# Kernel optimization log

Hardware: AMD Instinct MI355X
Metric: run time of the kernel (lower is better)

The kernel has to match this reference:

```python
import jax, jax.numpy as jnp
import numpy as np

N_NODES = 50000
N_EDGES = 800000
F_IN = 128
HEADS = 4
C = 64  # hidden_dim // heads
HIDDEN = HEADS * C
NUM_GRAPHS = 256
NEG_SLOPE = 0.2


def setup_inputs() -> dict:
    key = jax.random.key(0)
    ks = jax.random.split(key, 10)
    x = jax.random.normal(ks[0], (N_NODES, F_IN), dtype=jnp.float32)
    edge_index = jax.random.randint(ks[1], (2, N_EDGES), 0, N_NODES, dtype=jnp.int64)
    edge_attr = jax.random.normal(ks[2], (N_EDGES, 8), dtype=jnp.float32)
    batch = jnp.sort(jax.random.randint(ks[3], (N_NODES,), 0, NUM_GRAPHS, dtype=jnp.int64))
    # GATConv params (PyG: lin weight, att_src/att_dst, bias) + fc head
    W = jax.random.normal(ks[4], (F_IN, HIDDEN), dtype=jnp.float32) / np.sqrt(F_IN)
    att_src = jax.random.normal(ks[5], (HEADS, C), dtype=jnp.float32) / np.sqrt(C)
    att_dst = jax.random.normal(ks[6], (HEADS, C), dtype=jnp.float32) / np.sqrt(C)
    bias = jax.random.normal(ks[7], (HIDDEN,), dtype=jnp.float32) * 0.01
    fc_w = jax.random.normal(ks[8], (1, HIDDEN), dtype=jnp.float32) / np.sqrt(HIDDEN)
    fc_b = jax.random.normal(ks[9], (1,), dtype=jnp.float32) * 0.01
    return {"x": x, "edge_index": edge_index, "edge_attr": edge_attr, "batch": batch,
            "W": W, "att_src": att_src, "att_dst": att_dst, "bias": bias,
            "fc_w": fc_w, "fc_b": fc_b}


def reference(x, edge_index, edge_attr, batch, W, att_src, att_dst, bias, fc_w, fc_b):
    N = x.shape[0]
    # add self loops
    loops = jnp.arange(N, dtype=edge_index.dtype)
    src = jnp.concatenate([edge_index[0], loops])  # [E+N]
    dst = jnp.concatenate([edge_index[1], loops])
    # GATConv: linear transform per head
    h = (x @ W).reshape(N, HEADS, C)  # [N,H,C]
    a_src = jnp.einsum('nhc,hc->nh', h, att_src)  # [N,H]
    a_dst = jnp.einsum('nhc,hc->nh', h, att_dst)
    e = a_src[src] + a_dst[dst]  # [E,H]
    e = jnp.where(e > 0, e, NEG_SLOPE * e)  # leaky_relu
    # segment softmax over destination neighborhoods (self loops guarantee nonempty)
    m = jax.ops.segment_max(e, dst, num_segments=N)
    ee = jnp.exp(e - m[dst])
    s = jax.ops.segment_sum(ee, dst, num_segments=N)
    alpha = ee / s[dst]  # [E,H]
    msg = h[src] * alpha[:, :, None]  # [E,H,C]
    out = jax.ops.segment_sum(msg, dst, num_segments=N).reshape(N, HIDDEN) + bias
    out = jax.nn.elu(out)
    # global mean pool
    sums = jax.ops.segment_sum(out, batch, num_segments=NUM_GRAPHS)
    counts = jax.ops.segment_sum(jnp.ones((N,), out.dtype), batch, num_segments=NUM_GRAPHS)
    pooled = sums / jnp.maximum(counts, 1.0)[:, None]  # [G,HIDDEN]
    o = pooled @ fc_w.T + fc_b  # [G,1]
    return o.reshape(-1)
```

## Files before the change

### kernel.cpp

```cpp
#include <hip/hip_runtime.h>
#include <hip/hip_bf16.h>
#include <math.h>

#define HEADS   4
#define HIDDEN  256
#define FIN     128
#define NGRAPH  256
#define WPB     4

using frag_ab = __attribute__((ext_vector_type(8))) short;
using frag_cd = __attribute__((ext_vector_type(4))) float;

__device__ __forceinline__ float bf2f(unsigned short u) {
  union { unsigned int i; float f; } v; v.i = ((unsigned int)u) << 16; return v.f;
}
__device__ __forceinline__ unsigned short f2bf(float f) {
  union { float f; unsigned int i; } v; v.f = f;
  unsigned int b = v.i;
  b += 0x7FFFu + ((b >> 16) & 1u);
  return (unsigned short)(b >> 16);
}

__global__ __launch_bounds__(256) void k_prep(const float* __restrict__ W,
                                              unsigned short* __restrict__ Bf)
{
  int id = blockIdx.x * 256 + threadIdx.x;
  if (id >= 16 * 4 * 64) return;
  int l = id & 63, ks = (id >> 6) & 3, nfg = id >> 8;
  int col = nfg * 16 + (l & 15);
  int k0  = ks * 32 + (l >> 4) * 8;
  unsigned short v[8];
  #pragma unroll
  for (int j = 0; j < 8; ++j) v[j] = f2bf(W[(k0 + j) * HIDDEN + col]);
  *(uint4*)(Bf + (size_t)id * 8) = *(const uint4*)v;
}

__global__ __launch_bounds__(256) void k_gemm(
    const float* __restrict__ x, const unsigned short* __restrict__ Bf,
    const float* __restrict__ att_s, const float* __restrict__ att_d,
    unsigned short* __restrict__ h16, float* __restrict__ a_src, float* __restrict__ a_dst,
    int nNodes)
{
  __shared__ unsigned short As[32 * FIN];
  const int t  = threadIdx.x;
  const int n0 = blockIdx.x * 32;

  {
    const int row = t >> 3;
    const int g   = n0 + row;
    const int c0  = (t & 7) * 16;
    float4 f0, f1, f2, f3;
    if (g < nNodes) {
      const float* xr = x + (size_t)g * FIN + c0;
      f0 = *(const float4*)(xr + 0);  f1 = *(const float4*)(xr + 4);
      f2 = *(const float4*)(xr + 8);  f3 = *(const float4*)(xr + 12);
    } else {
      f0 = f1 = f2 = f3 = make_float4(0.f, 0.f, 0.f, 0.f);
    }
    unsigned short u[16];
    u[0]=f2bf(f0.x); u[1]=f2bf(f0.y); u[2]=f2bf(f0.z); u[3]=f2bf(f0.w);
    u[4]=f2bf(f1.x); u[5]=f2bf(f1.y); u[6]=f2bf(f1.z); u[7]=f2bf(f1.w);
    u[8]=f2bf(f2.x); u[9]=f2bf(f2.y); u[10]=f2bf(f2.z); u[11]=f2bf(f2.w);
    u[12]=f2bf(f3.x); u[13]=f2bf(f3.y); u[14]=f2bf(f3.z); u[15]=f2bf(f3.w);
    const int sw = (row & 7) << 4;
    char* base = (char*)As + row * 256;
    *(uint4*)(base + (((t & 7) * 32)      ^ sw)) = *(const uint4*)(u + 0);
    *(uint4*)(base + (((t & 7) * 32 + 16) ^ sw)) = *(const uint4*)(u + 8);
  }
  __syncthreads();

  const int w    = t >> 6;
  const int l    = t & 63;
  const int lrow = l & 15;

  frag_ab bfr[4][4];
  #pragma unroll
  for (int nf = 0; nf < 4; ++nf)
    #pragma unroll
    for (int ks = 0; ks < 4; ++ks)
      bfr[nf][ks] = *(const frag_ab*)(Bf + (size_t)(((w * 4 + nf) * 4 + ks) * 64 + l) * 8);

  frag_ab afr[2][4];
  const int lsw = (lrow & 7) << 4;
  #pragma unroll
  for (int mf = 0; mf < 2; ++mf)
    #pragma unroll
    for (int ks = 0; ks < 4; ++ks) {
      int byte = (mf * 16 + lrow) * 256 + ((ks * 64 + (l >> 4) * 16) ^ lsw);
      afr[mf][ks] = *(const frag_ab*)((const char*)As + byte);
    }

  frag_cd acc[2][4];
  #pragma unroll
  for (int mf = 0; mf < 2; ++mf)
    #pragma unroll
    for (int nf = 0; nf < 4; ++nf)
      acc[mf][nf] = (frag_cd){0.f, 0.f, 0.f, 0.f};
  #pragma unroll
  for (int ks = 0; ks < 4; ++ks)
    #pragma unroll
    for (int mf = 0; mf < 2; ++mf)
      #pragma unroll
      for (int nf = 0; nf < 4; ++nf)
        acc[mf][nf] = __builtin_amdgcn_mfma_f32_16x16x32_bf16(
            afr[mf][ks], bfr[nf][ks], acc[mf][nf], 0, 0, 0);

  float asw[4], adw[4];
  #pragma unroll
  for (int nf = 0; nf < 4; ++nf) {
    asw[nf] = att_s[w * 64 + nf * 16 + lrow];
    adw[nf] = att_d[w * 64 + nf * 16 + lrow];
  }

  #pragma unroll
  for (int mf = 0; mf < 2; ++mf) {
    #pragma unroll
    for (int r = 0; r < 4; ++r) {
      const int rowg = n0 + mf * 16 + (l >> 4) * 4 + r;
      if (rowg < nNodes) {
        #pragma unroll
        for (int nf = 0; nf < 4; ++nf)
          h16[(size_t)rowg * HIDDEN + w * 64 + nf * 16 + lrow] = f2bf(acc[mf][nf][r]);
      }
      float ss = 0.f, sd = 0.f;
      #pragma unroll
      for (int nf = 0; nf < 4; ++nf) {
        ss = fmaf(acc[mf][nf][r], asw[nf], ss);
        sd = fmaf(acc[mf][nf][r], adw[nf], sd);
      }
      #pragma unroll
      for (int off2 = 1; off2 <= 8; off2 <<= 1) {
        ss += __shfl_xor(ss, off2, 64);
        sd += __shfl_xor(sd, off2, 64);
      }
      if (lrow == 0 && rowg < nNodes) {
        a_src[rowg * HEADS + w] = ss;
        a_dst[rowg * HEADS + w] = sd;
      }
    }
  }
}

__global__ __launch_bounds__(256) void k_hist(const int* __restrict__ ei,
                                              int* __restrict__ count, int E, int N)
{
  int i = blockIdx.x * blockDim.x + threadIdx.x;
  int stride = gridDim.x * blockDim.x;
  for (int e = i; e < E; e += stride) atomicAdd(&count[ei[E + e]], 1);
  for (int n = i; n < N; n += stride) atomicAdd(&count[n], 1);
}

__global__ __launch_bounds__(256) void k_scan1(const int* __restrict__ cnt,
                                               int* __restrict__ offs,
                                               int* __restrict__ bsum, int n)
{
  int t = threadIdx.x, b = blockIdx.x;
  int i = b * 256 + t;
  int v = (i < n) ? cnt[i] : 0;
  int sc = v;
  #pragma unroll
  for (int d2 = 1; d2 < 64; d2 <<= 1) {
    int u = __shfl_up(sc, d2, 64);
    if ((t & 63) >= d2) sc += u;
  }
  __shared__ int wsum[4];
  if ((t & 63) == 63) wsum[t >> 6] = sc;
  __syncthreads();
  int base = 0;
  for (int w = 0; w < (t >> 6); ++w) base += wsum[w];
  int incl = sc + base;
  if (i < n) offs[i] = incl - v;
  if (t == 255) bsum[b] = incl;
}

__global__ __launch_bounds__(256) void k_scan2(const int* __restrict__ bsum,
                                               int* __restrict__ bsumo, int nb)
{
  int t = threadIdx.x;
  int v = (t < nb) ? bsum[t] : 0;
  int sc = v;
  #pragma unroll
  for (int d2 = 1; d2 < 64; d2 <<= 1) {
    int u = __shfl_up(sc, d2, 64);
    if ((t & 63) >= d2) sc += u;
  }
  __shared__ int wsum[4];
  if ((t & 63) == 63) wsum[t >> 6] = sc;
  __syncthreads();
  int base = 0;
  for (int w = 0; w < (t >> 6); ++w) base += wsum[w];
  int incl = sc + base;
  if (t < nb) bsumo[t] = incl - v;
}

__global__ __launch_bounds__(256) void k_scan3(int* __restrict__ offs,
                                               const int* __restrict__ bsumo,
                                               int* __restrict__ cursor, int n, int total)
{
  int t = threadIdx.x, b = blockIdx.x;
  int i = b * 256 + t;
  if (i < n) {
    int o = offs[i] + bsumo[b];
    offs[i] = o;
    cursor[i] = o;
  }
  if (i == 0) offs[n] = total;
}

__global__ __launch_bounds__(256) void k_scatter(
    const int* __restrict__ ei, int* __restrict__ cursor,
    int* __restrict__ ssrc, int E, int N)
{
  int e = blockIdx.x * 256 + threadIdx.x;
  int tot = E + N;
  if (e >= tot) return;
  int s, d;
  if (e < E) { s = ei[e]; d = ei[E + e]; }
  else       { s = e - E; d = s; }
  int pos = atomicAdd(&cursor[d], 1);
  ssrc[pos] = s;
}

__global__ __launch_bounds__(256) void k_agg(
    const unsigned short* __restrict__ h16, const int* __restrict__ offs,
    const int* __restrict__ ssrc,
    const float* __restrict__ a_src, const float* __restrict__ a_dst,
    const float* __restrict__ bias, const int* __restrict__ batch,
    unsigned short* __restrict__ outn, float* __restrict__ pooled, float* __restrict__ cntg,
    int N, int useAtomic)
{
  const int wid0 = blockIdx.x * WPB + (threadIdx.x >> 6);
  if (wid0 >= N) return;
  const int wid  = __builtin_amdgcn_readfirstlane(wid0);
  const int lane = threadIdx.x & 63;
  const int head = lane >> 4;
  const int col  = lane << 2;

  const int beg = offs[wid], end = offs[wid + 1];
  const float ad = a_dst[wid * 4 + head];

  float4 acc = make_float4(0.f, 0.f, 0.f, 0.f);
  float den = 0.f;
  int k = beg;

  for (; k + 8 <= end; k += 8) {
    int s0 = ssrc[k + 0], s1 = ssrc[k + 1], s2 = ssrc[k + 2], s3 = ssrc[k + 3];
    int s4 = ssrc[k + 4], s5 = ssrc[k + 5], s6 = ssrc[k + 6], s7 = ssrc[k + 7];
    float e0 = a_src[s0 * 4 + head], e1 = a_src[s1 * 4 + head];
    float e2 = a_src[s2 * 4 + head], e3 = a_src[s3 * 4 + head];
    float e4 = a_src[s4 * 4 + head], e5 = a_src[s5 * 4 + head];
    float e6 = a_src[s6 * 4 + head], e7 = a_src[s7 * 4 + head];
    ushort4 h0 = *(const ushort4*)(h16 + (size_t)s0 * HIDDEN + col);
    ushort4 h1 = *(const ushort4*)(h16 + (size_t)s1 * HIDDEN + col);
    ushort4 h2 = *(const ushort4*)(h16 + (size_t)s2 * HIDDEN + col);
    ushort4 h3 = *(const ushort4*)(h16 + (size_t)s3 * HIDDEN + col);
    ushort4 h4 = *(const ushort4*)(h16 + (size_t)s4 * HIDDEN + col);
    ushort4 h5 = *(const ushort4*)(h16 + (size_t)s5 * HIDDEN + col);
    ushort4 h6 = *(const ushort4*)(h16 + (size_t)s6 * HIDDEN + col);
    ushort4 h7 = *(const ushort4*)(h16 + (size_t)s7 * HIDDEN + col);
    float w0, w1, w2, w3, w4, w5, w6, w7;
    e0 += ad; e0 = e0 > 0.f ? e0 : 0.2f * e0; w0 = __expf(e0);
    e1 += ad; e1 = e1 > 0.f ? e1 : 0.2f * e1; w1 = __expf(e1);
    e2 += ad; e2 = e2 > 0.f ? e2 : 0.2f * e2; w2 = __expf(e2);
    e3 += ad; e3 = e3 > 0.f ? e3 : 0.2f * e3; w3 = __expf(e3);
    e4 += ad; e4 = e4 > 0.f ? e4 : 0.2f * e4; w4 = __expf(e4);
    e5 += ad; e5 = e5 > 0.f ? e5 : 0.2f * e5; w5 = __expf(e5);
    e6 += ad; e6 = e6 > 0.f ? e6 : 0.2f * e6; w6 = __expf(e6);
    e7 += ad; e7 = e7 > 0.f ? e7 : 0.2f * e7; w7 = __expf(e7);
    den += ((w0 + w1) + (w2 + w3)) + ((w4 + w5) + (w6 + w7));
    acc.x = fmaf(bf2f(h0.x), w0, acc.x); acc.y = fmaf(bf2f(h0.y), w0, acc.y);
    acc.z = fmaf(bf2f(h0.z), w0, acc.z); acc.w = fmaf(bf2f(h0.w), w0, acc.w);
    acc.x = fmaf(bf2f(h1.x), w1, acc.x); acc.y = fmaf(bf2f(h1.y), w1, acc.y);
    acc.z = fmaf(bf2f(h1.z), w1, acc.z); acc.w = fmaf(bf2f(h1.w), w1, acc.w);
    acc.x = fmaf(bf2f(h2.x), w2, acc.x); acc.y = fmaf(bf2f(h2.y), w2, acc.y);
    acc.z = fmaf(bf2f(h2.z), w2, acc.z); acc.w = fmaf(bf2f(h2.w), w2, acc.w);
    acc.x = fmaf(bf2f(h3.x), w3, acc.x); acc.y = fmaf(bf2f(h3.y), w3, acc.y);
    acc.z = fmaf(bf2f(h3.z), w3, acc.z); acc.w = fmaf(bf2f(h3.w), w3, acc.w);
    acc.x = fmaf(bf2f(h4.x), w4, acc.x); acc.y = fmaf(bf2f(h4.y), w4, acc.y);
    acc.z = fmaf(bf2f(h4.z), w4, acc.z); acc.w = fmaf(bf2f(h4.w), w4, acc.w);
    acc.x = fmaf(bf2f(h5.x), w5, acc.x); acc.y = fmaf(bf2f(h5.y), w5, acc.y);
    acc.z = fmaf(bf2f(h5.z), w5, acc.z); acc.w = fmaf(bf2f(h5.w), w5, acc.w);
    acc.x = fmaf(bf2f(h6.x), w6, acc.x); acc.y = fmaf(bf2f(h6.y), w6, acc.y);
    acc.z = fmaf(bf2f(h6.z), w6, acc.z); acc.w = fmaf(bf2f(h6.w), w6, acc.w);
    acc.x = fmaf(bf2f(h7.x), w7, acc.x); acc.y = fmaf(bf2f(h7.y), w7, acc.y);
    acc.z = fmaf(bf2f(h7.z), w7, acc.z); acc.w = fmaf(bf2f(h7.w), w7, acc.w);
  }
  for (; k < end; ++k) {
    int s = ssrc[k];
    float e = a_src[s * 4 + head] + ad;
    e = e > 0.f ? e : 0.2f * e;
    float w = __expf(e);
    ushort4 hv = *(const ushort4*)(h16 + (size_t)s * HIDDEN + col);
    den += w;
    acc.x = fmaf(bf2f(hv.x), w, acc.x); acc.y = fmaf(bf2f(hv.y), w, acc.y);
    acc.z = fmaf(bf2f(hv.z), w, acc.z); acc.w = fmaf(bf2f(hv.w), w, acc.w);
  }

  const float inv = 1.f / den;
  float4 bv = *(const float4*)&bias[col];
  float4 o;
  o.x = fmaf(acc.x, inv, bv.x); o.x = o.x > 0.f ? o.x : expm1f(o.x);
  o.y = fmaf(acc.y, inv, bv.y); o.y = o.y > 0.f ? o.y : expm1f(o.y);
  o.z = fmaf(acc.z, inv, bv.z); o.z = o.z > 0.f ? o.z : expm1f(o.z);
  o.w = fmaf(acc.w, inv, bv.w); o.w = o.w > 0.f ? o.w : expm1f(o.w);

  if (useAtomic) {
    int g = batch[wid];
    atomicAdd(&pooled[g * HIDDEN + col + 0], o.x);
    atomicAdd(&pooled[g * HIDDEN + col + 1], o.y);
    atomicAdd(&pooled[g * HIDDEN + col + 2], o.z);
    atomicAdd(&pooled[g * HIDDEN + col + 3], o.w);
    if (lane == 0) atomicAdd(&cntg[g], 1.0f);
  } else {
    ushort4 ov;
    ov.x = f2bf(o.x);
    ov.y = f2bf(o.y);
    ov.z = f2bf(o.z);
    ov.w = f2bf(o.w);
    *(ushort4*)(outn + (size_t)wid * HIDDEN + col) = ov;
  }
}

__global__ __launch_bounds__(256) void k_pool(
    const unsigned short* __restrict__ outn, const int* __restrict__ batch,
    const float* __restrict__ fc_w, const float* __restrict__ fc_b,
    float* __restrict__ out, int N)
{
  const int g = blockIdx.x, t = threadIdx.x;
  int a = 0, b = N;
  while (a < b) { int m = (a + b) >> 1; if (batch[m] < g) a = m + 1; else b = m; }
  const int lo = a;
  b = N;
  while (a < b) { int m = (a + b) >> 1; if (batch[m] < g + 1) a = m + 1; else b = m; }
  const int hi = a;

  float acc = 0.f, acc2 = 0.f;
  int n = lo;
  for (; n + 2 <= hi; n += 2) {
    acc  += bf2f(outn[(size_t)n * HIDDEN + t]);
    acc2 += bf2f(outn[(size_t)(n + 1) * HIDDEN + t]);
  }
  if (n < hi) acc += bf2f(outn[(size_t)n * HIDDEN + t]);
  acc += acc2;

  float cnt = (float)(hi - lo);
  float pooledv = acc / fmaxf(cnt, 1.0f);
  float v = pooledv * fc_w[t];
  #pragma unroll
  for (int off2 = 32; off2; off2 >>= 1) v += __shfl_xor(v, off2, 64);
  __shared__ float ws4[4];
  if ((t & 63) == 0) ws4[t >> 6] = v;
  __syncthreads();
  if (t == 0) out[g] = ws4[0] + ws4[1] + ws4[2] + ws4[3] + fc_b[0];
}

__global__ __launch_bounds__(64) void k_fc(
    const float* __restrict__ pooled, const float* __restrict__ cntg,
    const float* __restrict__ fc_w, const float* __restrict__ fc_b, float* __restrict__ out)
{
  int g = blockIdx.x, l = threadIdx.x;
  float acc = 0.f;
  for (int j = l; j < HIDDEN; j += 64) acc += pooled[g * HIDDEN + j] * fc_w[j];
  #pragma unroll
  for (int off2 = 32; off2; off2 >>= 1) acc += __shfl_xor(acc, off2, 64);
  if (l == 0) out[g] = acc / fmaxf(cntg[g], 1.0f) + fc_b[0];
}

extern "C" void kernel_launch(void* const* d_in, const int* in_sizes, int n_in,
                              void* d_out, int out_size, void* d_ws, size_t ws_size,
                              hipStream_t stream)
{
  const float* x     = (const float*)d_in[0];
  const int*   ei    = (const int*)  d_in[1];
  const int*   batch = (const int*)  d_in[3];
  const float* W     = (const float*)d_in[4];
  const float* att_s = (const float*)d_in[5];
  const float* att_d = (const float*)d_in[6];
  const float* bias  = (const float*)d_in[7];
  const float* fc_w  = (const float*)d_in[8];
  const float* fc_b  = (const float*)d_in[9];
  float* out = (float*)d_out;

  const int N   = in_sizes[0] / FIN;
  const int E   = in_sizes[1] / 2;
  const int TOT = E + N;

  char* p = (char*)d_ws;
  size_t o = 0;
  auto alloc = [&](size_t bytes) -> void* {
    void* r = p + o;
    o = (o + bytes + 255) & ~(size_t)255;
    return r;
  };
  int*   count  = (int*)  alloc((size_t)N * sizeof(int));
  float* pooled = (float*)alloc((size_t)NGRAPH * HIDDEN * sizeof(float));
  float* cntg   = (float*)alloc((size_t)NGRAPH * sizeof(float));
  size_t zeroBytes = o;
  unsigned short* h16 = (unsigned short*)alloc((size_t)N * HIDDEN * sizeof(unsigned short));
  unsigned short* Bf  = (unsigned short*)alloc((size_t)FIN * HIDDEN * sizeof(unsigned short));
  float* a_src  = (float*)alloc((size_t)N * 4 * sizeof(float));
  float* a_dst  = (float*)alloc((size_t)N * 4 * sizeof(float));
  int*   offs   = (int*)  alloc((size_t)(N + 1) * sizeof(int));
  int*   cursor = (int*)  alloc((size_t)N * sizeof(int));
  int*   bsum   = (int*)  alloc(1024);
  int*   bsumo  = (int*)  alloc(1024);
  int*   ssrc   = (int*)  alloc((size_t)TOT * sizeof(int));
  unsigned short* outn = (unsigned short*)alloc((size_t)N * HIDDEN * sizeof(unsigned short));
  const int useAtomic = (o > ws_size) ? 1 : 0;
  (void)n_in; (void)out_size;

  (void)hipMemsetAsync(d_ws, 0, zeroBytes, stream);

  hipLaunchKernelGGL(k_prep, dim3(16), dim3(256), 0, stream, W, Bf);
  hipLaunchKernelGGL(k_gemm, dim3((N + 31) / 32), dim3(256), 0, stream,
                     x, Bf, att_s, att_d, h16, a_src, a_dst, N);
  hipLaunchKernelGGL(k_hist, dim3(2048), dim3(256), 0, stream, ei, count, E, N);
  int sb = (N + 255) / 256;
  hipLaunchKernelGGL(k_scan1, dim3(sb), dim3(256), 0, stream, count, offs, bsum, N);
  hipLaunchKernelGGL(k_scan2, dim3(1), dim3(256), 0, stream, bsum, bsumo, sb);
  hipLaunchKernelGGL(k_scan3, dim3(sb), dim3(256), 0, stream, offs, bsumo, cursor, N, TOT);
  hipLaunchKernelGGL(k_scatter, dim3((TOT + 255) / 256), dim3(256), 0, stream,
                     ei, cursor, ssrc, E, N);
  hipLaunchKernelGGL(k_agg, dim3((N + WPB - 1) / WPB), dim3(256), 0, stream,
                     h16, offs, ssrc, a_src, a_dst, bias, batch,
                     outn, pooled, cntg, N, useAtomic);
  if (useAtomic) {
    hipLaunchKernelGGL(k_fc, dim3(NGRAPH), dim3(64), 0, stream,
                       pooled, cntg, fc_w, fc_b, out);
  } else {
    hipLaunchKernelGGL(k_pool, dim3(NGRAPH), dim3(256), 0, stream,
                       outn, batch, fc_w, fc_b, out, N);
  }
}
```

Baseline: 308.4 us.

## Fuse histogram into GEMM launch, merge scan passes, parallelize mean pooling

The edge-degree histogram now runs as extra blocks of the GEMM kernel, and the self-loop count is folded into the scan as +1 instead of separate atomics. The second and third scan passes are merged: each block sums the preceding block totals itself. The per-graph pooling kernel (256 blocks walking long node ranges) is replaced by a chunked pooling kernel that accumulates runs and flushes them with atomics, followed by the fc kernel. The aim is fewer launches and more parallel pooling, at the cost of extra float atomics and redundant block-sum reads in the scan.

```diff
diff --git a/kernel.cpp b/kernel.cpp
--- a/kernel.cpp
+++ b/kernel.cpp
@@ -7,6 +7,8 @@
 #define FIN     128
 #define NGRAPH  256
 #define WPB     4
+#define HISTB   512
+#define PCHUNK  64
 
 using frag_ab = __attribute__((ext_vector_type(8))) short;
 using frag_cd = __attribute__((ext_vector_type(4))) float;
@@ -35,14 +37,23 @@
   *(uint4*)(Bf + (size_t)id * 8) = *(const uint4*)v;
 }
 
-__global__ __launch_bounds__(256) void k_gemm(
+__global__ __launch_bounds__(256) void k_gemmhist(
     const float* __restrict__ x, const unsigned short* __restrict__ Bf,
     const float* __restrict__ att_s, const float* __restrict__ att_d,
     unsigned short* __restrict__ h16, float* __restrict__ a_src, float* __restrict__ a_dst,
-    int nNodes)
+    const int* __restrict__ ei, int* __restrict__ count,
+    int nNodes, int E, int gemmBlocks)
 {
   __shared__ unsigned short As[32 * FIN];
-  const int t  = threadIdx.x;
+  const int t = threadIdx.x;
+
+  if (blockIdx.x >= gemmBlocks) {
+    int i = (blockIdx.x - gemmBlocks) * 256 + t;
+    int stride = HISTB * 256;
+    for (int e = i; e < E; e += stride) atomicAdd(&count[ei[E + e]], 1);
+    return;
+  }
+
   const int n0 = blockIdx.x * 32;
 
   {
@@ -141,22 +152,13 @@
   }
 }
 
-__global__ __launch_bounds__(256) void k_hist(const int* __restrict__ ei,
-                                              int* __restrict__ count, int E, int N)
-{
-  int i = blockIdx.x * blockDim.x + threadIdx.x;
-  int stride = gridDim.x * blockDim.x;
-  for (int e = i; e < E; e += stride) atomicAdd(&count[ei[E + e]], 1);
-  for (int n = i; n < N; n += stride) atomicAdd(&count[n], 1);
-}
-
 __global__ __launch_bounds__(256) void k_scan1(const int* __restrict__ cnt,
                                                int* __restrict__ offs,
                                                int* __restrict__ bsum, int n)
 {
   int t = threadIdx.x, b = blockIdx.x;
   int i = b * 256 + t;
-  int v = (i < n) ? cnt[i] : 0;
+  int v = (i < n) ? cnt[i] + 1 : 0;
   int sc = v;
   #pragma unroll
   for (int d2 = 1; d2 < 64; d2 <<= 1) {
@@ -173,34 +175,25 @@
   if (t == 255) bsum[b] = incl;
 }
 
-__global__ __launch_bounds__(256) void k_scan2(const int* __restrict__ bsum,
-                                               int* __restrict__ bsumo, int nb)
-{
-  int t = threadIdx.x;
-  int v = (t < nb) ? bsum[t] : 0;
-  int sc = v;
-  #pragma unroll
-  for (int d2 = 1; d2 < 64; d2 <<= 1) {
-    int u = __shfl_up(sc, d2, 64);
-    if ((t & 63) >= d2) sc += u;
-  }
-  __shared__ int wsum[4];
-  if ((t & 63) == 63) wsum[t >> 6] = sc;
+__global__ __launch_bounds__(256) void k_scan23(int* __restrict__ offs,
+                                                const int* __restrict__ bsum,
+                                                int* __restrict__ cursor,
+                                                int n, int nb, int total)
+{
+  int t = threadIdx.x, b = blockIdx.x;
+  float dummy; (void)dummy;
+  int partial = 0;
+  for (int j = t; j < b; j += 256) partial += bsum[j];
+  #pragma unroll
+  for (int off2 = 32; off2; off2 >>= 1) partial += __shfl_xor(partial, off2, 64);
+  __shared__ int ws4[4];
+  if ((t & 63) == 0) ws4[t >> 6] = partial;
   __syncthreads();
-  int base = 0;
-  for (int w = 0; w < (t >> 6); ++w) base += wsum[w];
-  int incl = sc + base;
-  if (t < nb) bsumo[t] = incl - v;
-}
-
-__global__ __launch_bounds__(256) void k_scan3(int* __restrict__ offs,
-                                               const int* __restrict__ bsumo,
-                                               int* __restrict__ cursor, int n, int total)
-{
-  int t = threadIdx.x, b = blockIdx.x;
+  int blockBase = ws4[0] + ws4[1] + ws4[2] + ws4[3];
+
   int i = b * 256 + t;
   if (i < n) {
-    int o = offs[i] + bsumo[b];
+    int o = offs[i] + blockBase;
     offs[i] = o;
     cursor[i] = o;
   }
@@ -225,9 +218,8 @@
     const unsigned short* __restrict__ h16, const int* __restrict__ offs,
     const int* __restrict__ ssrc,
     const float* __restrict__ a_src, const float* __restrict__ a_dst,
-    const float* __restrict__ bias, const int* __restrict__ batch,
-    unsigned short* __restrict__ outn, float* __restrict__ pooled, float* __restrict__ cntg,
-    int N, int useAtomic)
+    const float* __restrict__ bias,
+    unsigned short* __restrict__ outn, int N)
 {
   const int wid0 = blockIdx.x * WPB + (threadIdx.x >> 6);
   if (wid0 >= N) return;
@@ -304,54 +296,58 @@
   o.z = fmaf(acc.z, inv, bv.z); o.z = o.z > 0.f ? o.z : expm1f(o.z);
   o.w = fmaf(acc.w, inv, bv.w); o.w = o.w > 0.f ? o.w : expm1f(o.w);
 
-  if (useAtomic) {
-    int g = batch[wid];
-    atomicAdd(&pooled[g * HIDDEN + col + 0], o.x);
-    atomicAdd(&pooled[g * HIDDEN + col + 1], o.y);
-    atomicAdd(&pooled[g * HIDDEN + col + 2], o.z);
-    atomicAdd(&pooled[g * HIDDEN + col + 3], o.w);
-    if (lane == 0) atomicAdd(&cntg[g], 1.0f);
-  } else {
-    ushort4 ov;
-    ov.x = f2bf(o.x);
-    ov.y = f2bf(o.y);
-    ov.z = f2bf(o.z);
-    ov.w = f2bf(o.w);
-    *(ushort4*)(outn + (size_t)wid * HIDDEN + col) = ov;
-  }
-}
-
-__global__ __launch_bounds__(256) void k_pool(
+  ushort4 ov;
+  ov.x = f2bf(o.x); ov.y = f2bf(o.y); ov.z = f2bf(o.z); ov.w = f2bf(o.w);
+  *(ushort4*)(outn + (size_t)wid * HIDDEN + col) = ov;
+}
+
+__global__ __launch_bounds__(256) void k_poolp(
     const unsigned short* __restrict__ outn, const int* __restrict__ batch,
-    const float* __restrict__ fc_w, const float* __restrict__ fc_b,
-    float* __restrict__ out, int N)
-{
-  const int g = blockIdx.x, t = threadIdx.x;
-  int a = 0, b = N;
-  while (a < b) { int m = (a + b) >> 1; if (batch[m] < g) a = m + 1; else b = m; }
-  const int lo = a;
-  b = N;
-  while (a < b) { int m = (a + b) >> 1; if (batch[m] < g + 1) a = m + 1; else b = m; }
-  const int hi = a;
-
-  float acc = 0.f, acc2 = 0.f;
-  int n = lo;
-  for (; n + 2 <= hi; n += 2) {
-    acc  += bf2f(outn[(size_t)n * HIDDEN + t]);
-    acc2 += bf2f(outn[(size_t)(n + 1) * HIDDEN + t]);
-  }
-  if (n < hi) acc += bf2f(outn[(size_t)n * HIDDEN + t]);
-  acc += acc2;
-
-  float cnt = (float)(hi - lo);
-  float pooledv = acc / fmaxf(cnt, 1.0f);
-  float v = pooledv * fc_w[t];
-  #pragma unroll
-  for (int off2 = 32; off2; off2 >>= 1) v += __shfl_xor(v, off2, 64);
-  __shared__ float ws4[4];
-  if ((t & 63) == 0) ws4[t >> 6] = v;
-  __syncthreads();
-  if (t == 0) out[g] = ws4[0] + ws4[1] + ws4[2] + ws4[3] + fc_b[0];
+    float* __restrict__ pooled, float* __restrict__ cntg, int N)
+{
+  const int t = threadIdx.x;
+  const int n0 = blockIdx.x * PCHUNK;
+  if (n0 >= N) return;
+  const int n1 = (n0 + PCHUNK < N) ? n0 + PCHUNK : N;
+
+  int cur = batch[n0];
+  float run = 0.f;
+  int runlen = 0;
+  int n = n0;
+  for (; n + 4 <= n1; n += 4) {
+    unsigned short r0 = outn[(size_t)(n + 0) * HIDDEN + t];
+    unsigned short r1 = outn[(size_t)(n + 1) * HIDDEN + t];
+    unsigned short r2 = outn[(size_t)(n + 2) * HIDDEN + t];
+    unsigned short r3 = outn[(size_t)(n + 3) * HIDDEN + t];
+    int g0 = batch[n + 0], g3 = batch[n + 3];
+    if (g0 == cur && g3 == cur) {
+      run += (bf2f(r0) + bf2f(r1)) + (bf2f(r2) + bf2f(r3));
+      runlen += 4;
+    } else {
+      unsigned short rr[4] = {r0, r1, r2, r3};
+      #pragma unroll
+      for (int j = 0; j < 4; ++j) {
+        int g = batch[n + j];
+        if (g != cur) {
+          atomicAdd(&pooled[cur * HIDDEN + t], run);
+          if (t == 0) atomicAdd(&cntg[cur], (float)runlen);
+          run = 0.f; runlen = 0; cur = g;
+        }
+        run += bf2f(rr[j]); runlen++;
+      }
+    }
+  }
+  for (; n < n1; ++n) {
+    int g = batch[n];
+    if (g != cur) {
+      atomicAdd(&pooled[cur * HIDDEN + t], run);
+      if (t == 0) atomicAdd(&cntg[cur], (float)runlen);
+      run = 0.f; runlen = 0; cur = g;
+    }
+    run += bf2f(outn[(size_t)n * HIDDEN + t]); runlen++;
+  }
+  atomicAdd(&pooled[cur * HIDDEN + t], run);
+  if (t == 0) atomicAdd(&cntg[cur], (float)runlen);
 }
 
 __global__ __launch_bounds__(64) void k_fc(
@@ -360,7 +356,8 @@
 {
   int g = blockIdx.x, l = threadIdx.x;
   float acc = 0.f;
-  for (int j = l; j < HIDDEN; j += 64) acc += pooled[g * HIDDEN + j] * fc_w[j];
+  #pragma unroll
+  for (int j = 0; j < HIDDEN / 64; ++j) acc += pooled[g * HIDDEN + j * 64 + l] * fc_w[j * 64 + l];
   #pragma unroll
   for (int off2 = 32; off2; off2 >>= 1) acc += __shfl_xor(acc, off2, 64);
   if (l == 0) out[g] = acc / fmaxf(cntg[g], 1.0f) + fc_b[0];
@@ -402,33 +399,26 @@
   float* a_dst  = (float*)alloc((size_t)N * 4 * sizeof(float));
   int*   offs   = (int*)  alloc((size_t)(N + 1) * sizeof(int));
   int*   cursor = (int*)  alloc((size_t)N * sizeof(int));
-  int*   bsum   = (int*)  alloc(1024);
-  int*   bsumo  = (int*)  alloc(1024);
+  int*   bsum   = (int*)  alloc(4096);
   int*   ssrc   = (int*)  alloc((size_t)TOT * sizeof(int));
   unsigned short* outn = (unsigned short*)alloc((size_t)N * HIDDEN * sizeof(unsigned short));
-  const int useAtomic = (o > ws_size) ? 1 : 0;
-  (void)n_in; (void)out_size;
+  (void)n_in; (void)out_size; (void)ws_size;
 
   (void)hipMemsetAsync(d_ws, 0, zeroBytes, stream);
 
+  const int gemmBlocks = (N + 31) / 32;
   hipLaunchKernelGGL(k_prep, dim3(16), dim3(256), 0, stream, W, Bf);
-  hipLaunchKernelGGL(k_gemm, dim3((N + 31) / 32), dim3(256), 0, stream,
-                     x, Bf, att_s, att_d, h16, a_src, a_dst, N);
-  hipLaunchKernelGGL(k_hist, dim3(2048), dim3(256), 0, stream, ei, count, E, N);
-  int sb = (N + 255) / 256;
+  hipLaunchKernelGGL(k_gemmhist, dim3(gemmBlocks + HISTB), dim3(256), 0, stream,
+                     x, Bf, att_s, att_d, h16, a_src, a_dst, ei, count, N, E, gemmBlocks);
+  const int sb = (N + 255) / 256;
   hipLaunchKernelGGL(k_scan1, dim3(sb), dim3(256), 0, stream, count, offs, bsum, N);
-  hipLaunchKernelGGL(k_scan2, dim3(1), dim3(256), 0, stream, bsum, bsumo, sb);
-  hipLaunchKernelGGL(k_scan3, dim3(sb), dim3(256), 0, stream, offs, bsumo, cursor, N, TOT);
+  hipLaunchKernelGGL(k_scan23, dim3(sb), dim3(256), 0, stream, offs, bsum, cursor, N, sb, TOT);
   hipLaunchKernelGGL(k_scatter, dim3((TOT + 255) / 256), dim3(256), 0, stream,
                      ei, cursor, ssrc, E, N);
   hipLaunchKernelGGL(k_agg, dim3((N + WPB - 1) / WPB), dim3(256), 0, stream,
-                     h16, offs, ssrc, a_src, a_dst, bias, batch,
-                     outn, pooled, cntg, N, useAtomic);
-  if (useAtomic) {
-    hipLaunchKernelGGL(k_fc, dim3(NGRAPH), dim3(64), 0, stream,
-                       pooled, cntg, fc_w, fc_b, out);
-  } else {
-    hipLaunchKernelGGL(k_pool, dim3(NGRAPH), dim3(256), 0, stream,
-                       outn, batch, fc_w, fc_b, out, N);
-  }
-}
+                     h16, offs, ssrc, a_src, a_dst, bias, outn, N);
+  hipLaunchKernelGGL(k_poolp, dim3((N + PCHUNK - 1) / PCHUNK), dim3(256), 0, stream,
+                     outn, batch, pooled, cntg, N);
+  hipLaunchKernelGGL(k_fc, dim3(NGRAPH), dim3(64), 0, stream,
+                     pooled, cntg, fc_w, fc_b, out);
+}
```

Result: faster. 276.9 us (-10.2%).
